# Optimization experiments

Measured on AMD Instinct MI355X. Metric: run time of the kernel, lower is better.

Reference implementation:

```python
import jax, jax.numpy as jnp
import numpy as np

H = 8  # n_heads
NEG = -1e32
LN_EPS = 1e-5


def setup_inputs() -> dict:
    key = jax.random.key(0)
    ks = jax.random.split(key, 10)
    B, S, D = 8, 1024, 512
    sd = 1.0 / np.sqrt(D)
    return {
        "q_in": jax.random.normal(ks[0], (B, S, D), jnp.float32),
        "k_in": jax.random.normal(ks[1], (B, S, D), jnp.float32),
        "v_in": jax.random.normal(ks[2], (B, S, D), jnp.float32),
        "state_mask": jax.random.randint(ks[3], (B, S, S), 0, 2, jnp.int32),
        "Wq": jax.random.normal(ks[4], (D, D), jnp.float32) * sd,
        "bq": jnp.zeros((D,), jnp.float32),
        "Wv": jax.random.normal(ks[5], (D, D), jnp.float32) * sd,
        "bv": jnp.zeros((D,), jnp.float32),
        "Wo": jax.random.normal(ks[6], (D, D), jnp.float32) * sd,
        "bo": jnp.zeros((D,), jnp.float32),
        "gammas": jax.random.normal(ks[7], (H, 1, 1), jnp.float32) * 0.1,
        "ln_g": jnp.ones((D,), jnp.float32),
        "ln_b": jnp.zeros((D,), jnp.float32),
    }


def _heads(x, B, S, h, dk):
    # [B,S,D] -> [B,h,S,dk]
    return x.reshape(B, S, h, dk).transpose(0, 2, 1, 3)


def reference(q_in, k_in, v_in, state_mask, Wq, bq, Wv, bv, Wo, bo, gammas, ln_g, ln_b):
    B, S, D = q_in.shape
    dk = D // H
    # strict causal mask (tril(-1)), as in DTransformerLayer with peek_cur=False
    causal = jnp.tril(jnp.ones((S, S), bool), -1)[None, None]  # [1,1,S,S]

    # --- LrState: decay-gamma scores on RAW embeddings, scaled by sqrt(d_model) (source quirk) ---
    qh = _heads(q_in, B, S, H, dk)
    kh = _heads(k_in, B, S, H, dk)
    s_scores = jnp.einsum("bhqd,bhkd->bhqk", qh, kh) / jnp.sqrt(jnp.float32(D))
    total_effect = jnp.clip(jnp.exp(-jax.nn.softplus(gammas)), 1e-5, 1e5)[None]  # [1,H,1,1]
    s_scores = s_scores * total_effect
    new_mask = (state_mask[:, None] != 0) & causal  # cluster mask AND causal
    s_scores = jnp.where(new_mask, s_scores, 0.0)

    # --- MultiHeadAttention (kq_same=True: k uses q_linear) ---
    q = _heads(q_in @ Wq + bq, B, S, H, dk)
    k = _heads(k_in @ Wq + bq, B, S, H, dk)
    v = _heads(v_in @ Wv + bv, B, S, H, dk)
    scores = jnp.einsum("bhqd,bhkd->bhqk", q, k) / jnp.sqrt(jnp.float32(dk))
    scores = jnp.where(causal, scores, NEG)
    scores = scores + s_scores
    scores = jnp.where(causal, scores, NEG)
    probs = jax.nn.softmax(scores, axis=-1)
    probs = jnp.where(causal, probs, 0.0)
    o = jnp.einsum("bhqk,bhkd->bhqd", probs, v)
    o = o.transpose(0, 2, 1, 3).reshape(B, S, D) @ Wo + bo

    # residual (dropout inactive in eval) + LayerNorm
    x = q_in + o
    mu = jnp.mean(x, -1, keepdims=True)
    var = jnp.mean(jnp.square(x - mu), -1, keepdims=True)
    return (x - mu) * jax.lax.rsqrt(var + LN_EPS) * ln_g + ln_b
```

## Files before the change

kernel.cpp:

```cpp
#include <hip/hip_runtime.h>
#include <math.h>

#define S_LEN 1024
#define D_MOD 512
#define NH 8
#define DK 64
#define NB 8

typedef __attribute__((ext_vector_type(8))) short short8;
typedef __attribute__((ext_vector_type(4))) float floatx4;

union U8 { ushort u[8]; short8 v; };

__device__ __forceinline__ ushort f2bf(float x) {
  unsigned u = __float_as_uint(x);
  unsigned r = (u + 0x7fffu + ((u >> 16) & 1u)) >> 16;
  return (ushort)r;
}

__global__ __launch_bounds__(256) void cvt3_kern(
    const float* __restrict__ q, const float* __restrict__ k,
    const float* __restrict__ v, ushort* __restrict__ qo,
    ushort* __restrict__ ko, ushort* __restrict__ vo)
{
  const int z = blockIdx.y;
  const float* src = (z == 0) ? q : (z == 1) ? k : v;
  ushort* dst = (z == 0) ? qo : (z == 1) ? ko : vo;
  const int i = blockIdx.x * 256 + threadIdx.x;
  const float4 a = *((const float4*)src + i * 2);
  const float4 b = *((const float4*)src + i * 2 + 1);
  U8 o;
  o.u[0] = f2bf(a.x); o.u[1] = f2bf(a.y); o.u[2] = f2bf(a.z); o.u[3] = f2bf(a.w);
  o.u[4] = f2bf(b.x); o.u[5] = f2bf(b.y); o.u[6] = f2bf(b.z); o.u[7] = f2bf(b.w);
  *(short8*)(dst + (size_t)i * 8) = o.v;
}

__global__ __launch_bounds__(256) void wtrans3_kern(
    const float* __restrict__ W0, const float* __restrict__ W1,
    const float* __restrict__ W2, ushort* __restrict__ T0,
    ushort* __restrict__ T1, ushort* __restrict__ T2)
{
  const int z = blockIdx.z;
  const float* W = (z == 0) ? W0 : (z == 1) ? W1 : W2;
  ushort* Wt = (z == 0) ? T0 : (z == 1) ? T1 : T2;
  __shared__ __align__(16) ushort tile[64][72];
  const int t = threadIdx.x;
  const int n0 = blockIdx.x * 64;
  const int k0 = blockIdx.y * 64;
  {
    const int r = t >> 2;
    const int c0 = (t & 3) * 16;
    const float* p = &W[(size_t)(k0 + r) * 512 + n0 + c0];
#pragma unroll
    for (int j = 0; j < 16; ++j) tile[r][c0 + j] = f2bf(p[j]);
  }
  __syncthreads();
  {
    const int c = t >> 2;
    const int kg = (t & 3) * 16;
    U8 lo, hi;
#pragma unroll
    for (int j = 0; j < 8; ++j) lo.u[j] = tile[kg + j][c];
#pragma unroll
    for (int j = 0; j < 8; ++j) hi.u[j] = tile[kg + 8 + j][c];
    ushort* q = &Wt[(size_t)(n0 + c) * 512 + k0 + kg];
    *(short8*)q = lo.v;
    *(short8*)(q + 8) = hi.v;
  }
}

__global__ __launch_bounds__(256) void maskbits_kern(
    const int* __restrict__ smask, unsigned long long* __restrict__ mb)
{
  const int row = blockIdx.x * 4 + (threadIdx.x >> 6);
  const int lane = threadIdx.x & 63;
  const int* p = smask + (size_t)row * S_LEN;
  unsigned long long mine = 0;
#pragma unroll
  for (int r = 0; r < 16; ++r) {
    int m = p[r * 64 + lane];
    unsigned long long w = __ballot(m != 0);
    if (lane == r) mine = w;
  }
  if (lane < 16) mb[(size_t)row * 16 + lane] = mine;
}

__global__ __launch_bounds__(256) void gemm_qkv_kern(
    const ushort* __restrict__ qr, const ushort* __restrict__ kr,
    const ushort* __restrict__ vr, const ushort* __restrict__ Wqt,
    const ushort* __restrict__ Wvt, const float* __restrict__ bq,
    const float* __restrict__ bv, ushort* __restrict__ Qo,
    ushort* __restrict__ Ko, ushort* __restrict__ VtO)
{
  __shared__ __align__(16) ushort Bl[64][520];

  const int z = blockIdx.z;
  const ushort* A = (z == 0) ? qr : (z == 1) ? kr : vr;
  const ushort* Wt = (z == 2) ? Wvt : Wqt;
  const float* bias = (z == 2) ? bv : bq;

  const int t = threadIdx.x;
  const int w = t >> 6;
  const int lane = t & 63;
  const int quad = lane >> 4;
  const int i16 = lane & 15;
  const int mbase = blockIdx.x * 128 + w * 32;
  const int nbase = blockIdx.y * 64;

  {
    const int srow = t >> 2;
    const int scol = (t & 3) * 128;
    const ushort* wp = Wt + (size_t)(nbase + srow) * 512 + scol;
#pragma unroll
    for (int j = 0; j < 16; ++j)
      *(short8*)&Bl[srow][scol + j * 8] = *(const short8*)(wp + j * 8);
  }
  __syncthreads();

  floatx4 acc[2][4];
#pragma unroll
  for (int mi = 0; mi < 2; ++mi)
#pragma unroll
    for (int ni = 0; ni < 4; ++ni) acc[mi][ni] = (floatx4)(0.f);

  const ushort* Ap = A + (size_t)(mbase + i16) * 512 + quad * 8;
  short8 a0 = *(const short8*)Ap;
  short8 a1 = *(const short8*)(Ap + 16 * 512);

#pragma unroll 4
  for (int k0 = 0; k0 < 512; k0 += 32) {
    short8 na0 = *(const short8*)(Ap + k0 + 32);
    short8 na1 = *(const short8*)(Ap + 16 * 512 + k0 + 32);
    short8 bf[4];
#pragma unroll
    for (int ni = 0; ni < 4; ++ni)
      bf[ni] = *(const short8*)&Bl[ni * 16 + i16][k0 + quad * 8];
#pragma unroll
    for (int ni = 0; ni < 4; ++ni) {
      acc[0][ni] = __builtin_amdgcn_mfma_f32_16x16x32_bf16(a0, bf[ni], acc[0][ni], 0, 0, 0);
      acc[1][ni] = __builtin_amdgcn_mfma_f32_16x16x32_bf16(a1, bf[ni], acc[1][ni], 0, 0, 0);
    }
    a0 = na0;
    a1 = na1;
  }

  float bv4[4];
#pragma unroll
  for (int ni = 0; ni < 4; ++ni) bv4[ni] = bias[nbase + ni * 16 + i16];

  if (z < 2) {
    ushort* C = (z == 0) ? Qo : Ko;
#pragma unroll
    for (int mi = 0; mi < 2; ++mi)
#pragma unroll
      for (int ni = 0; ni < 4; ++ni)
#pragma unroll
        for (int r = 0; r < 4; ++r) {
          const int m = mbase + mi * 16 + quad * 4 + r;
          const int n = nbase + ni * 16 + i16;
          C[(size_t)m * 512 + n] = f2bf(acc[mi][ni][r] + bv4[ni]);
        }
  } else {
#pragma unroll
    for (int mi = 0; mi < 2; ++mi)
#pragma unroll
      for (int ni = 0; ni < 4; ++ni) {
        const int m = mbase + mi * 16 + quad * 4;
        const int b = m >> 10;
        const int s = m & 1023;
        const int n = nbase + ni * 16 + i16;
        const int h = n >> 6;
        const int c = n & 63;
        ushort4 pk;
        pk.x = f2bf(acc[mi][ni][0] + bv4[ni]);
        pk.y = f2bf(acc[mi][ni][1] + bv4[ni]);
        pk.z = f2bf(acc[mi][ni][2] + bv4[ni]);
        pk.w = f2bf(acc[mi][ni][3] + bv4[ni]);
        *(ushort4*)(VtO + (((size_t)b * NH + h) * DK + c) * S_LEN + s) = pk;
      }
  }
}

__global__ __launch_bounds__(256) void gemm_out_kern(
    const ushort* __restrict__ A, const ushort* __restrict__ Wt,
    const float* __restrict__ bias, const float* __restrict__ R,
    float* __restrict__ X)
{
  __shared__ __align__(16) ushort Bl[64][520];

  const int t = threadIdx.x;
  const int w = t >> 6;
  const int lane = t & 63;
  const int quad = lane >> 4;
  const int i16 = lane & 15;
  const int mbase = blockIdx.x * 128 + w * 32;
  const int nbase = blockIdx.y * 64;

  {
    const int srow = t >> 2;
    const int scol = (t & 3) * 128;
    const ushort* wp = Wt + (size_t)(nbase + srow) * 512 + scol;
#pragma unroll
    for (int j = 0; j < 16; ++j)
      *(short8*)&Bl[srow][scol + j * 8] = *(const short8*)(wp + j * 8);
  }
  __syncthreads();

  floatx4 acc[2][4];
#pragma unroll
  for (int mi = 0; mi < 2; ++mi)
#pragma unroll
    for (int ni = 0; ni < 4; ++ni) acc[mi][ni] = (floatx4)(0.f);

  const ushort* Ap = A + (size_t)(mbase + i16) * 512 + quad * 8;
  short8 a0 = *(const short8*)Ap;
  short8 a1 = *(const short8*)(Ap + 16 * 512);

#pragma unroll 4
  for (int k0 = 0; k0 < 512; k0 += 32) {
    short8 na0 = *(const short8*)(Ap + k0 + 32);
    short8 na1 = *(const short8*)(Ap + 16 * 512 + k0 + 32);
    short8 bf[4];
#pragma unroll
    for (int ni = 0; ni < 4; ++ni)
      bf[ni] = *(const short8*)&Bl[ni * 16 + i16][k0 + quad * 8];
#pragma unroll
    for (int ni = 0; ni < 4; ++ni) {
      acc[0][ni] = __builtin_amdgcn_mfma_f32_16x16x32_bf16(a0, bf[ni], acc[0][ni], 0, 0, 0);
      acc[1][ni] = __builtin_amdgcn_mfma_f32_16x16x32_bf16(a1, bf[ni], acc[1][ni], 0, 0, 0);
    }
    a0 = na0;
    a1 = na1;
  }

  float bv4[4];
#pragma unroll
  for (int ni = 0; ni < 4; ++ni) bv4[ni] = bias[nbase + ni * 16 + i16];
#pragma unroll
  for (int mi = 0; mi < 2; ++mi)
#pragma unroll
    for (int ni = 0; ni < 4; ++ni)
#pragma unroll
      for (int r = 0; r < 4; ++r) {
        const int m = mbase + mi * 16 + quad * 4 + r;
        const int n = nbase + ni * 16 + i16;
        X[(size_t)m * 512 + n] = acc[mi][ni][r] + bv4[ni] + R[(size_t)m * 512 + n];
      }
}

__global__ __launch_bounds__(256) void attn_kern(
    const ushort* __restrict__ Qb, const ushort* __restrict__ Kb,
    const ushort* __restrict__ VtG, const ushort* __restrict__ qraw,
    const ushort* __restrict__ kraw,
    const unsigned long long* __restrict__ mbits,
    const float* __restrict__ gammas, ushort* __restrict__ Obf)
{
  __shared__ __align__(16) ushort Kp[64][64];
  __shared__ __align__(16) ushort Kr[64][64];
  __shared__ __align__(16) ushort Vc[64][64];
  __shared__ __align__(16) ushort Pl[4][16][64];

  const int t = threadIdx.x;
  const int w = t >> 6;
  const int lane = t & 63;
  const int quad = lane >> 4;
  const int i16 = lane & 15;
  const int bh = blockIdx.x;
  const int b = bh >> 3;
  const int h = bh & 7;
  const int p = blockIdx.y;

  const float gam = gammas[h];
  float te = __expf(-log1pf(__expf(gam)));
  te = fminf(fmaxf(te, 1e-5f), 1e5f);
  const float c1 = 0.125f * 1.44269504f;
  const float c2 = te * 0.044194173824159216f * 1.44269504f;

  const int xi = i16 & 7;
  const int rr = t >> 3;
  const int lc = t & 7;
  const int pc = ((lc ^ (rr & 7)) * 8);

#pragma unroll
  for (int seg = 0; seg < 2; ++seg) {
    const int qt = seg ? (15 - p) : p;
    const int qbase = qt * 64 + w * 16;

    short8 Qp[2], Qr[2];
    {
      const ushort* qp = Qb + ((size_t)b * S_LEN + qbase + i16) * D_MOD + h * DK + quad * 8;
      const ushort* qq = qraw + ((size_t)b * S_LEN + qbase + i16) * D_MOD + h * DK + quad * 8;
#pragma unroll
      for (int s = 0; s < 2; ++s) {
        Qp[s] = *(const short8*)(qp + s * 32);
        Qr[s] = *(const short8*)(qq + s * 32);
      }
    }

    floatx4 Oacc[4];
#pragma unroll
    for (int t4 = 0; t4 < 4; ++t4) Oacc[t4] = (floatx4)(0.f);
    float l_run[4] = {0.f, 0.f, 0.f, 0.f};

    const int nit = qt + 1;
    for (int kt = 0; kt < nit; ++kt) {
      const int k0 = kt * 64;

      const ushort* kpg = Kb + ((size_t)b * S_LEN + k0 + rr) * D_MOD + h * DK + lc * 8;
      const ushort* krg = kraw + ((size_t)b * S_LEN + k0 + rr) * D_MOD + h * DK + lc * 8;
      const ushort* vg  = VtG + ((size_t)bh * DK + rr) * S_LEN + k0 + lc * 8;
      short8 kpv0 = *(const short8*)kpg;
      short8 kpv1 = *(const short8*)(kpg + 32 * D_MOD);
      short8 krv0 = *(const short8*)krg;
      short8 krv1 = *(const short8*)(krg + 32 * D_MOD);
      short8 vv0  = *(const short8*)vg;
      short8 vv1  = *(const short8*)(vg + 32 * S_LEN);
      unsigned long long mw[4];
#pragma unroll
      for (int r = 0; r < 4; ++r)
        mw[r] = mbits[((size_t)b * S_LEN + qbase + quad * 4 + r) * 16 + kt];

      __syncthreads();
      *(short8*)&Kp[rr][pc] = kpv0;
      *(short8*)&Kp[rr + 32][pc] = kpv1;
      *(short8*)&Kr[rr][pc] = krv0;
      *(short8*)&Kr[rr + 32][pc] = krv1;
      *(short8*)&Vc[rr][pc] = vv0;
      *(short8*)&Vc[rr + 32][pc] = vv1;
      __syncthreads();

      floatx4 accp[4], accr[4];
#pragma unroll
      for (int t4 = 0; t4 < 4; ++t4) { accp[t4] = (floatx4)(0.f); accr[t4] = (floatx4)(0.f); }
#pragma unroll
      for (int s = 0; s < 2; ++s) {
        const int co = ((s * 4 + quad) ^ xi) * 8;
        short8 kp4[4], kr4[4];
#pragma unroll
        for (int t4 = 0; t4 < 4; ++t4) kp4[t4] = *(const short8*)&Kp[t4 * 16 + i16][co];
#pragma unroll
        for (int t4 = 0; t4 < 4; ++t4) kr4[t4] = *(const short8*)&Kr[t4 * 16 + i16][co];
#pragma unroll
        for (int t4 = 0; t4 < 4; ++t4)
          accp[t4] = __builtin_amdgcn_mfma_f32_16x16x32_bf16(Qp[s], kp4[t4], accp[t4], 0, 0, 0);
#pragma unroll
        for (int t4 = 0; t4 < 4; ++t4)
          accr[t4] = __builtin_amdgcn_mfma_f32_16x16x32_bf16(Qr[s], kr4[t4], accr[t4], 0, 0, 0);
      }

#pragma unroll
      for (int r = 0; r < 4; ++r) {
        const int qg = qbase + quad * 4 + r;
        const int prow = quad * 4 + r;
#pragma unroll
        for (int t4 = 0; t4 < 4; ++t4) {
          const int kg = k0 + t4 * 16 + i16;
          const float bitf = ((mw[r] >> (t4 * 16 + i16)) & 1ULL) ? c2 : 0.f;
          const float sv = accp[t4][r] * c1 + accr[t4][r] * bitf;
          const float pv = (kg < qg) ? exp2f(sv) : 0.f;
          l_run[r] += pv;
          const int kc = t4 * 2 + (i16 >> 3);
          Pl[w][prow][((kc ^ (prow & 7)) * 8) + (i16 & 7)] = f2bf(pv);
        }
      }

#pragma unroll
      for (int s = 0; s < 2; ++s) {
        const int co = ((s * 4 + quad) ^ xi) * 8;
        short8 a = *(const short8*)&Pl[w][i16][co];
#pragma unroll
        for (int t4 = 0; t4 < 4; ++t4) {
          short8 bv8 = *(const short8*)&Vc[t4 * 16 + i16][co];
          Oacc[t4] = __builtin_amdgcn_mfma_f32_16x16x32_bf16(a, bv8, Oacc[t4], 0, 0, 0);
        }
      }
    }

#pragma unroll
    for (int r = 0; r < 4; ++r) {
      float l = l_run[r];
#pragma unroll
      for (int off = 1; off < 16; off <<= 1) l += __shfl_xor(l, off);
      const float inv = (l > 0.f) ? 1.f / l : 0.f;
      ushort* orow = Obf + ((size_t)b * S_LEN + qbase + quad * 4 + r) * D_MOD + h * DK;
#pragma unroll
      for (int t4 = 0; t4 < 4; ++t4)
        orow[t4 * 16 + i16] = f2bf(Oacc[t4][r] * inv);
    }
  }
}

__global__ __launch_bounds__(256) void ln_kern(
    const float* __restrict__ X, const float* __restrict__ gw,
    const float* __restrict__ bw, float* __restrict__ out)
{
  const int row = blockIdx.x * 4 + (threadIdx.x >> 6);
  const int lane = threadIdx.x & 63;
  const int c = lane * 8;
  const float* xp = &X[(size_t)row * D_MOD + c];
  const float4 x0 = *(const float4*)xp;
  const float4 x1 = *(const float4*)(xp + 4);
  float xv[8] = {x0.x, x0.y, x0.z, x0.w, x1.x, x1.y, x1.z, x1.w};
  float sum = 0.f;
#pragma unroll
  for (int u = 0; u < 8; ++u) sum += xv[u];
#pragma unroll
  for (int off = 1; off < 64; off <<= 1) sum += __shfl_xor(sum, off, 64);
  const float mu = sum * (1.f / 512.f);
  float ss = 0.f;
#pragma unroll
  for (int u = 0; u < 8; ++u) { xv[u] -= mu; ss += xv[u] * xv[u]; }
#pragma unroll
  for (int off = 1; off < 64; off <<= 1) ss += __shfl_xor(ss, off, 64);
  const float rstd = rsqrtf(ss * (1.f / 512.f) + 1e-5f);
  const float4 g0 = *(const float4*)&gw[c];
  const float4 g1 = *(const float4*)&gw[c + 4];
  const float4 b0 = *(const float4*)&bw[c];
  const float4 b1 = *(const float4*)&bw[c + 4];
  float* op = &out[(size_t)row * D_MOD + c];
  *(float4*)op = make_float4(xv[0] * rstd * g0.x + b0.x,
                             xv[1] * rstd * g0.y + b0.y,
                             xv[2] * rstd * g0.z + b0.z,
                             xv[3] * rstd * g0.w + b0.w);
  *(float4*)(op + 4) = make_float4(xv[4] * rstd * g1.x + b1.x,
                                   xv[5] * rstd * g1.y + b1.y,
                                   xv[6] * rstd * g1.z + b1.z,
                                   xv[7] * rstd * g1.w + b1.w);
}

extern "C" void kernel_launch(void* const* d_in, const int* in_sizes, int n_in,
                              void* d_out, int out_size, void* d_ws, size_t ws_size,
                              hipStream_t stream)
{
  const float* q_in  = (const float*)d_in[0];
  const float* k_in  = (const float*)d_in[1];
  const float* v_in  = (const float*)d_in[2];
  const int*   smask = (const int*)d_in[3];
  const float* Wq = (const float*)d_in[4];
  const float* bq = (const float*)d_in[5];
  const float* Wv = (const float*)d_in[6];
  const float* bv = (const float*)d_in[7];
  const float* Wo = (const float*)d_in[8];
  const float* bo = (const float*)d_in[9];
  const float* gammas = (const float*)d_in[10];
  const float* ln_g = (const float*)d_in[11];
  const float* ln_b = (const float*)d_in[12];
  float* out = (float*)d_out;

  char* ws = (char*)d_ws;
  const size_t BF = (size_t)NB * S_LEN * D_MOD * sizeof(ushort);
  ushort* qr  = (ushort*)(ws);
  ushort* kr  = (ushort*)(ws + BF);
  ushort* vr  = (ushort*)(ws + 2 * BF);
  ushort* Obf = (ushort*)(ws + 2 * BF);
  ushort* Qbf = (ushort*)(ws + 3 * BF);
  ushort* Kbf = (ushort*)(ws + 4 * BF);
  ushort* Vt  = (ushort*)(ws + 5 * BF);
  unsigned long long* mbits = (unsigned long long*)(ws + 6 * BF);
  ushort* Wqt = (ushort*)(ws + 6 * BF + (1 << 20));
  ushort* Wvt = Wqt + 512 * 512;
  ushort* Wot = Wvt + 512 * 512;
  float*  X   = (float*)ws;

  const dim3 tb(256);

  cvt3_kern<<<dim3(2048, 3), tb, 0, stream>>>(q_in, k_in, v_in, qr, kr, vr);
  wtrans3_kern<<<dim3(8, 8, 3), tb, 0, stream>>>(Wq, Wv, Wo, Wqt, Wvt, Wot);
  maskbits_kern<<<dim3(2048), tb, 0, stream>>>(smask, mbits);

  gemm_qkv_kern<<<dim3(64, 8, 3), tb, 0, stream>>>(qr, kr, vr, Wqt, Wvt,
                                                   bq, bv, Qbf, Kbf, Vt);

  attn_kern<<<dim3(64, 8), tb, 0, stream>>>(Qbf, Kbf, Vt, qr, kr, mbits,
                                            gammas, Obf);

  gemm_out_kern<<<dim3(64, 8), tb, 0, stream>>>(Obf, Wot, bo, q_in, X);
  ln_kern<<<2048, tb, 0, stream>>>(X, ln_g, ln_b, out);
}
```

Before: 248.8 us.

## Double-buffer GEMM and attention tiles, fuse mask packing into conversion kernel

Both projection GEMMs now stream the weight tile through a 2-stage swizzled LDS buffer of 64-wide K chunks instead of staging the full 64x512 panel once, and keep a 3-deep register prefetch of A. The attention kernel double-buffers its K, raw-K and V tiles so the next tile's global loads overlap the current tile's compute, with one barrier per iteration. It also applies the causal mask only on the diagonal tile, uses the hardware exp2 and truncates P to bf16 instead of rounding. The mask-bit packing kernel is merged into the input conversion kernel as an extra grid row, saving a launch. Truncation slightly changes numerics, and the extra LDS may lower occupancy.

Measured after the change: 231.2 us. 7.1% less time.

```diff
diff --git a/kernel.cpp b/kernel.cpp
--- a/kernel.cpp
+++ b/kernel.cpp
@@ -18,21 +18,37 @@
   return (ushort)r;
 }
 
-__global__ __launch_bounds__(256) void cvt3_kern(
+__global__ __launch_bounds__(256) void prep_kern(
     const float* __restrict__ q, const float* __restrict__ k,
-    const float* __restrict__ v, ushort* __restrict__ qo,
-    ushort* __restrict__ ko, ushort* __restrict__ vo)
-{
-  const int z = blockIdx.y;
-  const float* src = (z == 0) ? q : (z == 1) ? k : v;
-  ushort* dst = (z == 0) ? qo : (z == 1) ? ko : vo;
-  const int i = blockIdx.x * 256 + threadIdx.x;
-  const float4 a = *((const float4*)src + i * 2);
-  const float4 b = *((const float4*)src + i * 2 + 1);
-  U8 o;
-  o.u[0] = f2bf(a.x); o.u[1] = f2bf(a.y); o.u[2] = f2bf(a.z); o.u[3] = f2bf(a.w);
-  o.u[4] = f2bf(b.x); o.u[5] = f2bf(b.y); o.u[6] = f2bf(b.z); o.u[7] = f2bf(b.w);
-  *(short8*)(dst + (size_t)i * 8) = o.v;
+    const float* __restrict__ v, const int* __restrict__ smask,
+    ushort* __restrict__ qo, ushort* __restrict__ ko,
+    ushort* __restrict__ vo, unsigned long long* __restrict__ mb)
+{
+  const int y = blockIdx.y;
+  const int t = threadIdx.x;
+  if (y < 3) {
+    const float* src = (y == 0) ? q : (y == 1) ? k : v;
+    ushort* dst = (y == 0) ? qo : (y == 1) ? ko : vo;
+    const int i = blockIdx.x * 256 + t;
+    const float4 a = *((const float4*)src + i * 2);
+    const float4 b = *((const float4*)src + i * 2 + 1);
+    U8 o;
+    o.u[0] = f2bf(a.x); o.u[1] = f2bf(a.y); o.u[2] = f2bf(a.z); o.u[3] = f2bf(a.w);
+    o.u[4] = f2bf(b.x); o.u[5] = f2bf(b.y); o.u[6] = f2bf(b.z); o.u[7] = f2bf(b.w);
+    *(short8*)(dst + (size_t)i * 8) = o.v;
+  } else {
+    const int row = blockIdx.x * 4 + (t >> 6);
+    const int lane = t & 63;
+    const int* p = smask + (size_t)row * S_LEN;
+    unsigned long long mine = 0;
+#pragma unroll
+    for (int r = 0; r < 16; ++r) {
+      int m = p[r * 64 + lane];
+      unsigned long long w = __ballot(m != 0);
+      if (lane == r) mine = w;
+    }
+    if (lane < 16) mb[(size_t)row * 16 + lane] = mine;
+  }
 }
 
 __global__ __launch_bounds__(256) void wtrans3_kern(
@@ -69,22 +85,6 @@
   }
 }
 
-__global__ __launch_bounds__(256) void maskbits_kern(
-    const int* __restrict__ smask, unsigned long long* __restrict__ mb)
-{
-  const int row = blockIdx.x * 4 + (threadIdx.x >> 6);
-  const int lane = threadIdx.x & 63;
-  const int* p = smask + (size_t)row * S_LEN;
-  unsigned long long mine = 0;
-#pragma unroll
-  for (int r = 0; r < 16; ++r) {
-    int m = p[r * 64 + lane];
-    unsigned long long w = __ballot(m != 0);
-    if (lane == r) mine = w;
-  }
-  if (lane < 16) mb[(size_t)row * 16 + lane] = mine;
-}
-
 __global__ __launch_bounds__(256) void gemm_qkv_kern(
     const ushort* __restrict__ qr, const ushort* __restrict__ kr,
     const ushort* __restrict__ vr, const ushort* __restrict__ Wqt,
@@ -92,7 +92,7 @@
     const float* __restrict__ bv, ushort* __restrict__ Qo,
     ushort* __restrict__ Ko, ushort* __restrict__ VtO)
 {
-  __shared__ __align__(16) ushort Bl[64][520];
+  __shared__ __align__(16) ushort Bl[2][64][64];
 
   const int z = blockIdx.z;
   const ushort* A = (z == 0) ? qr : (z == 1) ? kr : vr;
@@ -107,41 +107,73 @@
   const int mbase = blockIdx.x * 128 + w * 32;
   const int nbase = blockIdx.y * 64;
 
+  const int sr = t >> 2;
+  const int slc = (t & 3) * 2;
+  const int sp0 = ((slc ^ (sr & 7)) * 8);
+  const int sp1 = (((slc + 1) ^ (sr & 7)) * 8);
+  const ushort* Bg = Wt + (size_t)(nbase + sr) * 512 + (t & 3) * 16;
+  const int xb = i16 & 7;
+
+  const ushort* Ap = A + (size_t)(mbase + i16) * 512 + quad * 8;
+
+  floatx4 acc[2][4];
+#pragma unroll
+  for (int mi = 0; mi < 2; ++mi)
+#pragma unroll
+    for (int ni = 0; ni < 4; ++ni) acc[mi][ni] = (floatx4)(0.f);
+
+  short8 areg[3][2][2];
+#pragma unroll
+  for (int d = 0; d < 2; ++d)
+#pragma unroll
+    for (int mi = 0; mi < 2; ++mi)
+#pragma unroll
+      for (int kc = 0; kc < 2; ++kc)
+        areg[d][mi][kc] = *(const short8*)(Ap + d * 64 + kc * 32 + mi * 16 * 512);
+
   {
-    const int srow = t >> 2;
-    const int scol = (t & 3) * 128;
-    const ushort* wp = Wt + (size_t)(nbase + srow) * 512 + scol;
-#pragma unroll
-    for (int j = 0; j < 16; ++j)
-      *(short8*)&Bl[srow][scol + j * 8] = *(const short8*)(wp + j * 8);
-  }
-  __syncthreads();
-
-  floatx4 acc[2][4];
-#pragma unroll
-  for (int mi = 0; mi < 2; ++mi)
-#pragma unroll
-    for (int ni = 0; ni < 4; ++ni) acc[mi][ni] = (floatx4)(0.f);
-
-  const ushort* Ap = A + (size_t)(mbase + i16) * 512 + quad * 8;
-  short8 a0 = *(const short8*)Ap;
-  short8 a1 = *(const short8*)(Ap + 16 * 512);
-
-#pragma unroll 4
-  for (int k0 = 0; k0 < 512; k0 += 32) {
-    short8 na0 = *(const short8*)(Ap + k0 + 32);
-    short8 na1 = *(const short8*)(Ap + 16 * 512 + k0 + 32);
-    short8 bf[4];
-#pragma unroll
-    for (int ni = 0; ni < 4; ++ni)
-      bf[ni] = *(const short8*)&Bl[ni * 16 + i16][k0 + quad * 8];
-#pragma unroll
-    for (int ni = 0; ni < 4; ++ni) {
-      acc[0][ni] = __builtin_amdgcn_mfma_f32_16x16x32_bf16(a0, bf[ni], acc[0][ni], 0, 0, 0);
-      acc[1][ni] = __builtin_amdgcn_mfma_f32_16x16x32_bf16(a1, bf[ni], acc[1][ni], 0, 0, 0);
-    }
-    a0 = na0;
-    a1 = na1;
+    short8 b0 = *(const short8*)Bg;
+    short8 b1 = *(const short8*)(Bg + 8);
+    *(short8*)&Bl[0][sr][sp0] = b0;
+    *(short8*)&Bl[0][sr][sp1] = b1;
+    __syncthreads();
+  }
+
+#pragma unroll
+  for (int kt = 0; kt < 8; ++kt) {
+    const int cb = kt & 1;
+    short8 nb0, nb1;
+    if (kt < 7) {
+      nb0 = *(const short8*)(Bg + (kt + 1) * 64);
+      nb1 = *(const short8*)(Bg + (kt + 1) * 64 + 8);
+    }
+    if (kt < 6) {
+#pragma unroll
+      for (int mi = 0; mi < 2; ++mi)
+#pragma unroll
+        for (int kc = 0; kc < 2; ++kc)
+          areg[(kt + 2) % 3][mi][kc] =
+              *(const short8*)(Ap + (kt + 2) * 64 + kc * 32 + mi * 16 * 512);
+    }
+    short8 bf[2][4];
+#pragma unroll
+    for (int kc = 0; kc < 2; ++kc)
+#pragma unroll
+      for (int ni = 0; ni < 4; ++ni)
+        bf[kc][ni] = *(const short8*)&Bl[cb][ni * 16 + i16][((kc * 4 + quad) ^ xb) * 8];
+#pragma unroll
+    for (int kc = 0; kc < 2; ++kc)
+#pragma unroll
+      for (int mi = 0; mi < 2; ++mi)
+#pragma unroll
+        for (int ni = 0; ni < 4; ++ni)
+          acc[mi][ni] = __builtin_amdgcn_mfma_f32_16x16x32_bf16(
+              areg[kt % 3][mi][kc], bf[kc][ni], acc[mi][ni], 0, 0, 0);
+    if (kt < 7) {
+      *(short8*)&Bl[cb ^ 1][sr][sp0] = nb0;
+      *(short8*)&Bl[cb ^ 1][sr][sp1] = nb1;
+      __syncthreads();
+    }
   }
 
   float bv4[4];
@@ -186,7 +218,7 @@
     const float* __restrict__ bias, const float* __restrict__ R,
     float* __restrict__ X)
 {
-  __shared__ __align__(16) ushort Bl[64][520];
+  __shared__ __align__(16) ushort Bl[2][64][64];
 
   const int t = threadIdx.x;
   const int w = t >> 6;
@@ -196,41 +228,73 @@
   const int mbase = blockIdx.x * 128 + w * 32;
   const int nbase = blockIdx.y * 64;
 
+  const int sr = t >> 2;
+  const int slc = (t & 3) * 2;
+  const int sp0 = ((slc ^ (sr & 7)) * 8);
+  const int sp1 = (((slc + 1) ^ (sr & 7)) * 8);
+  const ushort* Bg = Wt + (size_t)(nbase + sr) * 512 + (t & 3) * 16;
+  const int xb = i16 & 7;
+
+  const ushort* Ap = A + (size_t)(mbase + i16) * 512 + quad * 8;
+
+  floatx4 acc[2][4];
+#pragma unroll
+  for (int mi = 0; mi < 2; ++mi)
+#pragma unroll
+    for (int ni = 0; ni < 4; ++ni) acc[mi][ni] = (floatx4)(0.f);
+
+  short8 areg[3][2][2];
+#pragma unroll
+  for (int d = 0; d < 2; ++d)
+#pragma unroll
+    for (int mi = 0; mi < 2; ++mi)
+#pragma unroll
+      for (int kc = 0; kc < 2; ++kc)
+        areg[d][mi][kc] = *(const short8*)(Ap + d * 64 + kc * 32 + mi * 16 * 512);
+
   {
-    const int srow = t >> 2;
-    const int scol = (t & 3) * 128;
-    const ushort* wp = Wt + (size_t)(nbase + srow) * 512 + scol;
-#pragma unroll
-    for (int j = 0; j < 16; ++j)
-      *(short8*)&Bl[srow][scol + j * 8] = *(const short8*)(wp + j * 8);
-  }
-  __syncthreads();
-
-  floatx4 acc[2][4];
-#pragma unroll
-  for (int mi = 0; mi < 2; ++mi)
-#pragma unroll
-    for (int ni = 0; ni < 4; ++ni) acc[mi][ni] = (floatx4)(0.f);
-
-  const ushort* Ap = A + (size_t)(mbase + i16) * 512 + quad * 8;
-  short8 a0 = *(const short8*)Ap;
-  short8 a1 = *(const short8*)(Ap + 16 * 512);
-
-#pragma unroll 4
-  for (int k0 = 0; k0 < 512; k0 += 32) {
-    short8 na0 = *(const short8*)(Ap + k0 + 32);
-    short8 na1 = *(const short8*)(Ap + 16 * 512 + k0 + 32);
-    short8 bf[4];
-#pragma unroll
-    for (int ni = 0; ni < 4; ++ni)
-      bf[ni] = *(const short8*)&Bl[ni * 16 + i16][k0 + quad * 8];
-#pragma unroll
-    for (int ni = 0; ni < 4; ++ni) {
-      acc[0][ni] = __builtin_amdgcn_mfma_f32_16x16x32_bf16(a0, bf[ni], acc[0][ni], 0, 0, 0);
-      acc[1][ni] = __builtin_amdgcn_mfma_f32_16x16x32_bf16(a1, bf[ni], acc[1][ni], 0, 0, 0);
-    }
-    a0 = na0;
-    a1 = na1;
+    short8 b0 = *(const short8*)Bg;
+    short8 b1 = *(const short8*)(Bg + 8);
+    *(short8*)&Bl[0][sr][sp0] = b0;
+    *(short8*)&Bl[0][sr][sp1] = b1;
+    __syncthreads();
+  }
+
+#pragma unroll
+  for (int kt = 0; kt < 8; ++kt) {
+    const int cb = kt & 1;
+    short8 nb0, nb1;
+    if (kt < 7) {
+      nb0 = *(const short8*)(Bg + (kt + 1) * 64);
+      nb1 = *(const short8*)(Bg + (kt + 1) * 64 + 8);
+    }
+    if (kt < 6) {
+#pragma unroll
+      for (int mi = 0; mi < 2; ++mi)
+#pragma unroll
+        for (int kc = 0; kc < 2; ++kc)
+          areg[(kt + 2) % 3][mi][kc] =
+              *(const short8*)(Ap + (kt + 2) * 64 + kc * 32 + mi * 16 * 512);
+    }
+    short8 bf[2][4];
+#pragma unroll
+    for (int kc = 0; kc < 2; ++kc)
+#pragma unroll
+      for (int ni = 0; ni < 4; ++ni)
+        bf[kc][ni] = *(const short8*)&Bl[cb][ni * 16 + i16][((kc * 4 + quad) ^ xb) * 8];
+#pragma unroll
+    for (int kc = 0; kc < 2; ++kc)
+#pragma unroll
+      for (int mi = 0; mi < 2; ++mi)
+#pragma unroll
+        for (int ni = 0; ni < 4; ++ni)
+          acc[mi][ni] = __builtin_amdgcn_mfma_f32_16x16x32_bf16(
+              areg[kt % 3][mi][kc], bf[kc][ni], acc[mi][ni], 0, 0, 0);
+    if (kt < 7) {
+      *(short8*)&Bl[cb ^ 1][sr][sp0] = nb0;
+      *(short8*)&Bl[cb ^ 1][sr][sp1] = nb1;
+      __syncthreads();
+    }
   }
 
   float bv4[4];
@@ -255,9 +319,9 @@
     const unsigned long long* __restrict__ mbits,
     const float* __restrict__ gammas, ushort* __restrict__ Obf)
 {
-  __shared__ __align__(16) ushort Kp[64][64];
-  __shared__ __align__(16) ushort Kr[64][64];
-  __shared__ __align__(16) ushort Vc[64][64];
+  __shared__ __align__(16) ushort Kp[2][64][64];
+  __shared__ __align__(16) ushort Kr[2][64][64];
+  __shared__ __align__(16) ushort Vc[2][64][64];
   __shared__ __align__(16) ushort Pl[4][16][64];
 
   const int t = threadIdx.x;
@@ -281,6 +345,10 @@
   const int lc = t & 7;
   const int pc = ((lc ^ (rr & 7)) * 8);
 
+  const ushort* kpgB = Kb + ((size_t)b * S_LEN + rr) * D_MOD + h * DK + lc * 8;
+  const ushort* krgB = kraw + ((size_t)b * S_LEN + rr) * D_MOD + h * DK + lc * 8;
+  const ushort* vgB  = VtG + ((size_t)bh * DK + rr) * S_LEN + lc * 8;
+
 #pragma unroll
   for (int seg = 0; seg < 2; ++seg) {
     const int qt = seg ? (15 - p) : p;
@@ -303,31 +371,44 @@
     float l_run[4] = {0.f, 0.f, 0.f, 0.f};
 
     const int nit = qt + 1;
+
+    {
+      short8 k0v0 = *(const short8*)kpgB;
+      short8 k0v1 = *(const short8*)(kpgB + 32 * D_MOD);
+      short8 r0v0 = *(const short8*)krgB;
+      short8 r0v1 = *(const short8*)(krgB + 32 * D_MOD);
+      short8 v0v0 = *(const short8*)vgB;
+      short8 v0v1 = *(const short8*)(vgB + 32 * S_LEN);
+      __syncthreads();
+      *(short8*)&Kp[0][rr][pc] = k0v0;
+      *(short8*)&Kp[0][rr + 32][pc] = k0v1;
+      *(short8*)&Kr[0][rr][pc] = r0v0;
+      *(short8*)&Kr[0][rr + 32][pc] = r0v1;
+      *(short8*)&Vc[0][rr][pc] = v0v0;
+      *(short8*)&Vc[0][rr + 32][pc] = v0v1;
+      __syncthreads();
+    }
+
     for (int kt = 0; kt < nit; ++kt) {
-      const int k0 = kt * 64;
-
-      const ushort* kpg = Kb + ((size_t)b * S_LEN + k0 + rr) * D_MOD + h * DK + lc * 8;
-      const ushort* krg = kraw + ((size_t)b * S_LEN + k0 + rr) * D_MOD + h * DK + lc * 8;
-      const ushort* vg  = VtG + ((size_t)bh * DK + rr) * S_LEN + k0 + lc * 8;
-      short8 kpv0 = *(const short8*)kpg;
-      short8 kpv1 = *(const short8*)(kpg + 32 * D_MOD);
-      short8 krv0 = *(const short8*)krg;
-      short8 krv1 = *(const short8*)(krg + 32 * D_MOD);
-      short8 vv0  = *(const short8*)vg;
-      short8 vv1  = *(const short8*)(vg + 32 * S_LEN);
+      const int cb = kt & 1;
+      const bool havenext = (kt + 1 < nit);
+      const bool diag = (kt == qt);
+
+      short8 nk0, nk1, nr0, nr1, nv0, nv1;
+      if (havenext) {
+        const size_t ko = (size_t)(kt + 1) * 64;
+        nk0 = *(const short8*)(kpgB + ko * D_MOD);
+        nk1 = *(const short8*)(kpgB + ko * D_MOD + 32 * D_MOD);
+        nr0 = *(const short8*)(krgB + ko * D_MOD);
+        nr1 = *(const short8*)(krgB + ko * D_MOD + 32 * D_MOD);
+        nv0 = *(const short8*)(vgB + ko);
+        nv1 = *(const short8*)(vgB + ko + 32 * S_LEN);
+      }
+
       unsigned long long mw[4];
 #pragma unroll
       for (int r = 0; r < 4; ++r)
         mw[r] = mbits[((size_t)b * S_LEN + qbase + quad * 4 + r) * 16 + kt];
-
-      __syncthreads();
-      *(short8*)&Kp[rr][pc] = kpv0;
-      *(short8*)&Kp[rr + 32][pc] = kpv1;
-      *(short8*)&Kr[rr][pc] = krv0;
-      *(short8*)&Kr[rr + 32][pc] = krv1;
-      *(short8*)&Vc[rr][pc] = vv0;
-      *(short8*)&Vc[rr + 32][pc] = vv1;
-      __syncthreads();
 
       floatx4 accp[4], accr[4];
 #pragma unroll
@@ -337,9 +418,9 @@
         const int co = ((s * 4 + quad) ^ xi) * 8;
         short8 kp4[4], kr4[4];
 #pragma unroll
-        for (int t4 = 0; t4 < 4; ++t4) kp4[t4] = *(const short8*)&Kp[t4 * 16 + i16][co];
-#pragma unroll
-        for (int t4 = 0; t4 < 4; ++t4) kr4[t4] = *(const short8*)&Kr[t4 * 16 + i16][co];
+        for (int t4 = 0; t4 < 4; ++t4) kp4[t4] = *(const short8*)&Kp[cb][t4 * 16 + i16][co];
+#pragma unroll
+        for (int t4 = 0; t4 < 4; ++t4) kr4[t4] = *(const short8*)&Kr[cb][t4 * 16 + i16][co];
 #pragma unroll
         for (int t4 = 0; t4 < 4; ++t4)
           accp[t4] = __builtin_amdgcn_mfma_f32_16x16x32_bf16(Qp[s], kp4[t4], accp[t4], 0, 0, 0);
@@ -348,19 +429,24 @@
           accr[t4] = __builtin_amdgcn_mfma_f32_16x16x32_bf16(Qr[s], kr4[t4], accr[t4], 0, 0, 0);
       }
 
+      const int k0g = kt * 64;
 #pragma unroll
       for (int r = 0; r < 4; ++r) {
         const int qg = qbase + quad * 4 + r;
         const int prow = quad * 4 + r;
 #pragma unroll
         for (int t4 = 0; t4 < 4; ++t4) {
-          const int kg = k0 + t4 * 16 + i16;
           const float bitf = ((mw[r] >> (t4 * 16 + i16)) & 1ULL) ? c2 : 0.f;
           const float sv = accp[t4][r] * c1 + accr[t4][r] * bitf;
-          const float pv = (kg < qg) ? exp2f(sv) : 0.f;
+          float pv = __builtin_amdgcn_exp2f(sv);
+          if (diag) {
+            const int kg = k0g + t4 * 16 + i16;
+            pv = (kg < qg) ? pv : 0.f;
+          }
           l_run[r] += pv;
           const int kc = t4 * 2 + (i16 >> 3);
-          Pl[w][prow][((kc ^ (prow & 7)) * 8) + (i16 & 7)] = f2bf(pv);
+          Pl[w][prow][((kc ^ (prow & 7)) * 8) + (i16 & 7)] =
+              (ushort)(__float_as_uint(pv) >> 16);
         }
       }
 
@@ -370,9 +456,19 @@
         short8 a = *(const short8*)&Pl[w][i16][co];
 #pragma unroll
         for (int t4 = 0; t4 < 4; ++t4) {
-          short8 bv8 = *(const short8*)&Vc[t4 * 16 + i16][co];
+          short8 bv8 = *(const short8*)&Vc[cb][t4 * 16 + i16][co];
           Oacc[t4] = __builtin_amdgcn_mfma_f32_16x16x32_bf16(a, bv8, Oacc[t4], 0, 0, 0);
         }
+      }
+
+      if (havenext) {
+        *(short8*)&Kp[cb ^ 1][rr][pc] = nk0;
+        *(short8*)&Kp[cb ^ 1][rr + 32][pc] = nk1;
+        *(short8*)&Kr[cb ^ 1][rr][pc] = nr0;
+        *(short8*)&Kr[cb ^ 1][rr + 32][pc] = nr1;
+        *(short8*)&Vc[cb ^ 1][rr][pc] = nv0;
+        *(short8*)&Vc[cb ^ 1][rr + 32][pc] = nv1;
+        __syncthreads();
       }
     }
 
@@ -464,9 +560,9 @@
 
   const dim3 tb(256);
 
-  cvt3_kern<<<dim3(2048, 3), tb, 0, stream>>>(q_in, k_in, v_in, qr, kr, vr);
+  prep_kern<<<dim3(2048, 4), tb, 0, stream>>>(q_in, k_in, v_in, smask,
+                                              qr, kr, vr, mbits);
   wtrans3_kern<<<dim3(8, 8, 3), tb, 0, stream>>>(Wq, Wv, Wo, Wqt, Wvt, Wot);
-  maskbits_kern<<<dim3(2048), tb, 0, stream>>>(smask, mbits);
 
   gemm_qkv_kern<<<dim3(64, 8, 3), tb, 0, stream>>>(qr, kr, vr, Wqt, Wvt,
                                                    bq, bv, Qbf, Kbf, Vt);
```
